# Kernel tuning notes

Hardware: AMD Instinct MI355X
Metric: run time of the kernel (lower is better)

Reference implementation:

```python
import jax, jax.numpy as jnp
import numpy as np

EPS = 1e-8
Q_MAX = 127.0  # 2**(8-1) - 1


def _activation_quant(x):
    gamma = jnp.maximum(jnp.max(jnp.abs(x)), EPS)
    scale = Q_MAX / gamma
    x_int = jnp.clip(jnp.round(x * scale), -Q_MAX, Q_MAX)
    x_fq = x_int / scale
    # straight-through estimator
    return x + jax.lax.stop_gradient(x_fq - x)


def _weight_quant(w):
    gamma = jnp.maximum(jnp.mean(jnp.abs(w)), EPS)
    w_int = jnp.clip(jnp.round(w / gamma), -1.0, 1.0)
    w_fq = w_int * gamma
    return w + jax.lax.stop_gradient(w_fq - w)


def setup_inputs() -> dict:
    key = jax.random.key(0)
    kx, kw, kb = jax.random.split(key, 3)
    in_features, out_features = 2048, 2048
    x = jax.random.normal(kx, (4, 4096, in_features), dtype=jnp.float32)
    # nn.Linear default init: U(-1/sqrt(fan_in), 1/sqrt(fan_in))
    bound = 1.0 / np.sqrt(in_features)
    W = jax.random.uniform(kw, (out_features, in_features), dtype=jnp.float32,
                           minval=-bound, maxval=bound)
    b = jax.random.uniform(kb, (out_features,), dtype=jnp.float32,
                           minval=-bound, maxval=bound)
    return {"x": x, "W": W, "b": b}


def reference(x, W, b):
    x_q = _activation_quant(x)          # int8 absmax fake-quant
    w_q = _weight_quant(W)              # ternary {-g, 0, g} fake-quant
    # F.linear: x @ W^T + b
    return jnp.einsum('bsi,oi->bso', x_q, w_q) + b
```

## Files before the change

### kernel.cpp

```cpp
#include <hip/hip_runtime.h>
#include <hip/hip_bf16.h>
#include <stdint.h>

typedef __attribute__((ext_vector_type(4))) int i32x4;

static constexpr long M_ = 16384;
static constexpr long N_ = 2048;
static constexpr long K_ = 2048;


#define GLOAD_LDS16(g, l)                                                          \
  __builtin_amdgcn_global_load_lds(                                               \
      (const __attribute__((address_space(1))) unsigned int*)(g),                 \
      (__attribute__((address_space(3))) unsigned int*)(l), 16, 0, 0)

__global__ __launch_bounds__(256) void k_stats(const float4* __restrict__ x,
                                               const float4* __restrict__ w,
                                               unsigned* __restrict__ gx_bits,
                                               double* __restrict__ gw_sum) {
  const int b = blockIdx.x;
  const int lane = threadIdx.x & 63, wv = threadIdx.x >> 6;
  if (b < 2048) {
    const long S = 524288;
    long i = (long)b * 256 + threadIdx.x;
    float m0 = 0.f, m1 = 0.f;
#pragma unroll
    for (int it = 0; it < 8; ++it) {
      float4 v0 = x[i];
      float4 v1 = x[i + S];
      m0 = fmaxf(m0, fmaxf(fmaxf(fabsf(v0.x), fabsf(v0.y)), fmaxf(fabsf(v0.z), fabsf(v0.w))));
      m1 = fmaxf(m1, fmaxf(fmaxf(fabsf(v1.x), fabsf(v1.y)), fmaxf(fabsf(v1.z), fabsf(v1.w))));
      i += 2 * S;
    }
    float m = fmaxf(m0, m1);
#pragma unroll
    for (int off = 32; off > 0; off >>= 1) m = fmaxf(m, __shfl_down(m, off));
    __shared__ float sm[4];
    if (lane == 0) sm[wv] = m;
    __syncthreads();
    if (threadIdx.x == 0) {
      float bm = fmaxf(fmaxf(sm[0], sm[1]), fmaxf(sm[2], sm[3]));
      atomicMax(gx_bits, __float_as_uint(bm));
    }
  } else {
    const long S = 131072;
    long i = (long)(b - 2048) * 256 + threadIdx.x;
    double s = 0.0;
#pragma unroll
    for (int it = 0; it < 8; ++it) {
      float4 v = w[i];
      s += (double)fabsf(v.x) + (double)fabsf(v.y) + (double)fabsf(v.z) + (double)fabsf(v.w);
      i += S;
    }
#pragma unroll
    for (int off = 32; off > 0; off >>= 1) s += __shfl_down(s, off);
    __shared__ double sd[4];
    if (lane == 0) sd[wv] = s;
    __syncthreads();
    if (threadIdx.x == 0) atomicAdd(gw_sum, (sd[0] + sd[1]) + (sd[2] + sd[3]));
  }
}

__global__ __launch_bounds__(256) void k_quant(const float4* __restrict__ x,
                                               const float4* __restrict__ w,
                                               char4* __restrict__ xq,
                                               char4* __restrict__ wq,
                                               const unsigned* __restrict__ gx_bits,
                                               const double* __restrict__ gw_sum) {
  const int b = blockIdx.x;
  if (b < 2048) {
    const double gx = (double)fmaxf(__uint_as_float(*gx_bits), 1e-8f);
    const double scale = 127.0 / gx;
    const long S = 524288;
    long i = (long)b * 256 + threadIdx.x;
#pragma unroll
    for (int it = 0; it < 16; ++it) {
      float4 v = x[i];
      char4 o;
      o.x = (signed char)(int)fmin(fmax(rint((double)v.x * scale), -127.0), 127.0);
      o.y = (signed char)(int)fmin(fmax(rint((double)v.y * scale), -127.0), 127.0);
      o.z = (signed char)(int)fmin(fmax(rint((double)v.z * scale), -127.0), 127.0);
      o.w = (signed char)(int)fmin(fmax(rint((double)v.w * scale), -127.0), 127.0);
      xq[i] = o;
      i += S;
    }
  } else {
    const double gw = fmax(*gw_sum * (1.0 / 4194304.0), 1e-8);
    const double inv = 1.0 / gw;
    const long S = 131072;
    long i = (long)(b - 2048) * 256 + threadIdx.x;
#pragma unroll
    for (int it = 0; it < 8; ++it) {
      float4 v = w[i];
      char4 o;
      o.x = (signed char)(int)fmin(fmax(rint((double)v.x * inv), -1.0), 1.0);
      o.y = (signed char)(int)fmin(fmax(rint((double)v.y * inv), -1.0), 1.0);
      o.z = (signed char)(int)fmin(fmax(rint((double)v.z * inv), -1.0), 1.0);
      o.w = (signed char)(int)fmin(fmax(rint((double)v.w * inv), -1.0), 1.0);
      wq[i] = o;
      i += S;
    }
  }
}


template <int ISB, int BUF, int KS>
__device__ __forceinline__ void stage2(signed char* lds, const signed char* gp, int kb,
                                       int go0, int ldsl0) {
  constexpr int R = ISB * 65536 + BUF * 32768 + KS * 16384;
  GLOAD_LDS16(gp + kb + go0, lds + R + ldsl0);
  GLOAD_LDS16(gp + kb + go0 + 32768, lds + R + ldsl0 + 1024);
}

template <int BUF, int KS, int MH, int SGB, int SGBUF, int SGKS, int VM>
__device__ __forceinline__ void phase(signed char* lds, const signed char* Ap,
                                      const signed char* Bp, int kb,
                                      const signed char* pA, const signed char* pB,
                                      int go0, int ldsl0, i32x4 acc[8][4], i32x4 b4[4]) {
  constexpr int RB = BUF * 32768 + KS * 16384;
  constexpr int RA = RB + MH * 4096;
  i32x4 a4[4];
  if (MH == 0) {
#pragma unroll
    for (int n = 0; n < 4; ++n) b4[n] = *(const i32x4*)(pB + RB + n * 1024);
  }
#pragma unroll
  for (int mm = 0; mm < 4; ++mm) a4[mm] = *(const i32x4*)(pA + RA + mm * 1024);

  if (SGB)
    stage2<1, SGBUF, SGKS>(lds, Bp, kb, go0, ldsl0);
  else
    stage2<0, SGBUF, SGKS>(lds, Ap, kb, go0, ldsl0);

  __builtin_amdgcn_s_barrier();
  asm volatile("s_waitcnt lgkmcnt(0)" ::: "memory");
  __builtin_amdgcn_s_setprio(1);
#pragma unroll
  for (int mm = 0; mm < 4; ++mm)
#pragma unroll
    for (int n = 0; n < 4; ++n)
      acc[MH * 4 + mm][n] =
          __builtin_amdgcn_mfma_i32_16x16x64_i8(a4[mm], b4[n], acc[MH * 4 + mm][n], 0, 0, 0);
  __builtin_amdgcn_s_setprio(0);
  if (VM) asm volatile("s_waitcnt vmcnt(8)" ::: "memory");
  __builtin_amdgcn_s_barrier();
}

__global__ __launch_bounds__(512, 2) void k_gemm(
    const signed char* __restrict__ Aq, const signed char* __restrict__ Bq,
    const float* __restrict__ bias, float* __restrict__ out,
    const unsigned* __restrict__ gx_bits, const double* __restrict__ gw_sum) {
  extern __shared__ signed char lds[];

  const int tid = threadIdx.x;
  const int lane = tid & 63;
  const int wid = tid >> 6;
  const int wave_m = wid >> 2;
  const int wave_n = wid & 3;
  const int l15 = lane & 15;

  const int wg = (int)((blockIdx.x & 7) * 64 + (blockIdx.x >> 3));
  const int nblk = wg & 7;
  const int mblk = wg >> 3;
  const long brow = (long)mblk * 256;
  const long bcol = (long)nblk * 256;

  const signed char* Ap = Aq + brow * K_;
  const signed char* Bp = Bq + bcol * K_;

  const int swz = ((lane >> 4) ^ ((l15 >> 1) & 3)) << 4;
  const signed char* pA = lds + (wave_m * 128 + l15) * 64 + swz;
  const signed char* pB = lds + 65536 + (wave_n * 64 + l15) * 64 + swz;

  const int c0 = (lane & 3) ^ ((lane >> 3) & 3);
  const int go0 = (wid * 32 + (lane >> 2)) * (int)K_ + c0 * 16;
  const int ldsl0 = wid * 2048;

  i32x4 acc[8][4];
#pragma unroll
  for (int m = 0; m < 8; m++)
#pragma unroll
    for (int n = 0; n < 4; n++) acc[m][n] = (i32x4){0, 0, 0, 0};
  i32x4 b4[4];

  stage2<0, 0, 0>(lds, Ap, 0, go0, ldsl0);
  stage2<1, 0, 0>(lds, Bp, 0, go0, ldsl0);
  stage2<0, 0, 1>(lds, Ap, 64, go0, ldsl0);
  stage2<1, 0, 1>(lds, Bp, 64, go0, ldsl0);
  stage2<0, 1, 0>(lds, Ap, 128, go0, ldsl0);
  stage2<1, 1, 0>(lds, Bp, 128, go0, ldsl0);
  asm volatile("s_waitcnt vmcnt(0)" ::: "memory");
  __builtin_amdgcn_s_barrier();

  for (int kt = 0; kt < (int)K_; kt += 256) {
    const int k1h = (kt + 192) & 2047;
    const int k2 = (kt + 256) & 2047;
    const int k3 = (kt + 384) & 2047;
    phase<0, 0, 0, 0, 1, 1, 0>(lds, Ap, Bp, k1h, pA, pB, go0, ldsl0, acc, b4);
    phase<0, 0, 1, 1, 1, 1, 1>(lds, Ap, Bp, k1h, pA, pB, go0, ldsl0, acc, b4);
    phase<0, 1, 0, 0, 0, 0, 0>(lds, Ap, Bp, k2, pA, pB, go0, ldsl0, acc, b4);
    phase<0, 1, 1, 1, 0, 0, 1>(lds, Ap, Bp, k2, pA, pB, go0, ldsl0, acc, b4);
    phase<1, 0, 0, 0, 0, 1, 0>(lds, Ap, Bp, k2 + 64, pA, pB, go0, ldsl0, acc, b4);
    phase<1, 0, 1, 1, 0, 1, 1>(lds, Ap, Bp, k2 + 64, pA, pB, go0, ldsl0, acc, b4);
    phase<1, 1, 0, 0, 1, 0, 0>(lds, Ap, Bp, k3, pA, pB, go0, ldsl0, acc, b4);
    phase<1, 1, 1, 1, 1, 0, 1>(lds, Ap, Bp, k3, pA, pB, go0, ldsl0, acc, b4);
  }

  const float gxf = fmaxf(__uint_as_float(*gx_bits), 1e-8f);
  const double gwd = fmax(*gw_sum * (1.0 / 4194304.0), 1e-8);
  const float alpha = (float)((double)gxf * gwd * (1.0 / 127.0));

#pragma unroll
  for (int n = 0; n < 4; ++n) {
    const long col = bcol + wave_n * 64 + n * 16 + l15;
    const float bv = bias[col];
#pragma unroll
    for (int m = 0; m < 8; ++m) {
      const long row0 = brow + wave_m * 128 + m * 16 + (lane >> 4) * 4;
#pragma unroll
      for (int r = 0; r < 4; ++r) {
        out[(row0 + r) * N_ + col] = (float)acc[m][n][r] * alpha + bv;
      }
    }
  }
}

extern "C" void kernel_launch(void* const* d_in, const int* in_sizes, int n_in,
                              void* d_out, int out_size, void* d_ws, size_t ws_size,
                              hipStream_t stream) {
  const float* x = (const float*)d_in[0];
  const float* W = (const float*)d_in[1];
  const float* b = (const float*)d_in[2];
  float* out = (float*)d_out;

  char* ws = (char*)d_ws;
  double* gw_sum = (double*)ws;
  unsigned* gx_bits = (unsigned*)(ws + 8);
  signed char* xq = (signed char*)(ws + 256);
  signed char* wq = (signed char*)(ws + 256 + (size_t)M_ * (size_t)K_);

  static bool attr_set = false;
  if (!attr_set) {
    (void)hipFuncSetAttribute(reinterpret_cast<const void*>(&k_gemm),
                              hipFuncAttributeMaxDynamicSharedMemorySize, 131072);
    attr_set = true;
  }

  hipMemsetAsync(ws, 0, 16, stream);
  hipLaunchKernelGGL(k_stats, dim3(2560), dim3(256), 0, stream,
                     (const float4*)x, (const float4*)W, gx_bits, gw_sum);
  hipLaunchKernelGGL(k_quant, dim3(2560), dim3(256), 0, stream,
                     (const float4*)x, (const float4*)W, (char4*)xq, (char4*)wq,
                     gx_bits, gw_sum);
  hipLaunchKernelGGL(k_gemm, dim3((unsigned)((M_ / 256) * (N_ / 256))), dim3(512),
                     131072, stream, xq, wq, b, out, gx_bits, gw_sum);
}
```

Baseline: 153.8 us.

## Merge half-phases into one phase per k-slice with 32 MFMAs between barriers

Replaces the two half-phases per k-slice (each loading B, four A fragments, one async stage and 16 MFMAs between barriers) with one phase that loads all 12 LDS fragments, issues both A and B async stages, then runs 32 MFMAs. This halves the barrier and wait count per k-slice and gives each MFMA burst more work to hide latency. It drops the explicit lgkmcnt wait, leaving the compiler to insert it, adds a sched_barrier, and raises register pressure from holding eight A fragments at once.

New measurement: 155.7 us. No clear change (+1.2%).

```diff
diff --git a/kernel.cpp b/kernel.cpp
--- a/kernel.cpp
+++ b/kernel.cpp
@@ -112,38 +112,40 @@
   GLOAD_LDS16(gp + kb + go0 + 32768, lds + R + ldsl0 + 1024);
 }
 
-template <int BUF, int KS, int MH, int SGB, int SGBUF, int SGKS, int VM>
-__device__ __forceinline__ void phase(signed char* lds, const signed char* Ap,
-                                      const signed char* Bp, int kb,
-                                      const signed char* pA, const signed char* pB,
-                                      int go0, int ldsl0, i32x4 acc[8][4], i32x4 b4[4]) {
+template <int BUF, int KS, int SGBUF, int SGKS>
+__device__ __forceinline__ void pairphase(signed char* lds, const signed char* Ap,
+                                          const signed char* Bp, int kb,
+                                          const signed char* pA, const signed char* pB,
+                                          int go0, int ldsl0, i32x4 acc[8][4]) {
   constexpr int RB = BUF * 32768 + KS * 16384;
-  constexpr int RA = RB + MH * 4096;
-  i32x4 a4[4];
-  if (MH == 0) {
-#pragma unroll
-    for (int n = 0; n < 4; ++n) b4[n] = *(const i32x4*)(pB + RB + n * 1024);
-  }
-#pragma unroll
-  for (int mm = 0; mm < 4; ++mm) a4[mm] = *(const i32x4*)(pA + RA + mm * 1024);
-
-  if (SGB)
-    stage2<1, SGBUF, SGKS>(lds, Bp, kb, go0, ldsl0);
-  else
-    stage2<0, SGBUF, SGKS>(lds, Ap, kb, go0, ldsl0);
+  i32x4 b4[4], alo[4], ahi[4];
+#pragma unroll
+  for (int n = 0; n < 4; ++n) b4[n] = *(const i32x4*)(pB + RB + n * 1024);
+#pragma unroll
+  for (int m = 0; m < 4; ++m) alo[m] = *(const i32x4*)(pA + RB + m * 1024);
+#pragma unroll
+  for (int m = 0; m < 4; ++m) ahi[m] = *(const i32x4*)(pA + RB + 4096 + m * 1024);
+
+  stage2<0, SGBUF, SGKS>(lds, Ap, kb, go0, ldsl0);
+  stage2<1, SGBUF, SGKS>(lds, Bp, kb, go0, ldsl0);
 
   __builtin_amdgcn_s_barrier();
-  asm volatile("s_waitcnt lgkmcnt(0)" ::: "memory");
   __builtin_amdgcn_s_setprio(1);
 #pragma unroll
-  for (int mm = 0; mm < 4; ++mm)
+  for (int m = 0; m < 4; ++m)
 #pragma unroll
     for (int n = 0; n < 4; ++n)
-      acc[MH * 4 + mm][n] =
-          __builtin_amdgcn_mfma_i32_16x16x64_i8(a4[mm], b4[n], acc[MH * 4 + mm][n], 0, 0, 0);
+      acc[m][n] = __builtin_amdgcn_mfma_i32_16x16x64_i8(alo[m], b4[n], acc[m][n], 0, 0, 0);
+#pragma unroll
+  for (int m = 0; m < 4; ++m)
+#pragma unroll
+    for (int n = 0; n < 4; ++n)
+      acc[4 + m][n] =
+          __builtin_amdgcn_mfma_i32_16x16x64_i8(ahi[m], b4[n], acc[4 + m][n], 0, 0, 0);
   __builtin_amdgcn_s_setprio(0);
-  if (VM) asm volatile("s_waitcnt vmcnt(8)" ::: "memory");
+  asm volatile("s_waitcnt vmcnt(8)" ::: "memory");
   __builtin_amdgcn_s_barrier();
+  __builtin_amdgcn_sched_barrier(0);
 }
 
 __global__ __launch_bounds__(512, 2) void k_gemm(
@@ -181,7 +183,6 @@
   for (int m = 0; m < 8; m++)
 #pragma unroll
     for (int n = 0; n < 4; n++) acc[m][n] = (i32x4){0, 0, 0, 0};
-  i32x4 b4[4];
 
   stage2<0, 0, 0>(lds, Ap, 0, go0, ldsl0);
   stage2<1, 0, 0>(lds, Bp, 0, go0, ldsl0);
@@ -196,14 +197,10 @@
     const int k1h = (kt + 192) & 2047;
     const int k2 = (kt + 256) & 2047;
     const int k3 = (kt + 384) & 2047;
-    phase<0, 0, 0, 0, 1, 1, 0>(lds, Ap, Bp, k1h, pA, pB, go0, ldsl0, acc, b4);
-    phase<0, 0, 1, 1, 1, 1, 1>(lds, Ap, Bp, k1h, pA, pB, go0, ldsl0, acc, b4);
-    phase<0, 1, 0, 0, 0, 0, 0>(lds, Ap, Bp, k2, pA, pB, go0, ldsl0, acc, b4);
-    phase<0, 1, 1, 1, 0, 0, 1>(lds, Ap, Bp, k2, pA, pB, go0, ldsl0, acc, b4);
-    phase<1, 0, 0, 0, 0, 1, 0>(lds, Ap, Bp, k2 + 64, pA, pB, go0, ldsl0, acc, b4);
-    phase<1, 0, 1, 1, 0, 1, 1>(lds, Ap, Bp, k2 + 64, pA, pB, go0, ldsl0, acc, b4);
-    phase<1, 1, 0, 0, 1, 0, 0>(lds, Ap, Bp, k3, pA, pB, go0, ldsl0, acc, b4);
-    phase<1, 1, 1, 1, 1, 0, 1>(lds, Ap, Bp, k3, pA, pB, go0, ldsl0, acc, b4);
+    pairphase<0, 0, 1, 1>(lds, Ap, Bp, k1h, pA, pB, go0, ldsl0, acc);
+    pairphase<0, 1, 0, 0>(lds, Ap, Bp, k2, pA, pB, go0, ldsl0, acc);
+    pairphase<1, 0, 0, 1>(lds, Ap, Bp, k2 + 64, pA, pB, go0, ldsl0, acc);
+    pairphase<1, 1, 1, 0>(lds, Ap, Bp, k3, pA, pB, go0, ldsl0, acc);
   }
 
   const float gxf = fmaxf(__uint_as_float(*gx_bits), 1e-8f);
```
